# Kernel tuning notes

Hardware: AMD Instinct MI355X
Metric: run time of the kernel (lower is better)

## Reference

```python
import jax, jax.numpy as jnp
import numpy as np

NUM_FEATURES = 768
HIDDEN = 1024
BATCH = 8192
K = 32


def setup_inputs() -> dict:
    key = jax.random.key(0)
    k1, k2, k3, k4, k5 = jax.random.split(key, 5)
    white_features = jax.random.randint(k1, (BATCH, K), 0, NUM_FEATURES, dtype=jnp.int64 if jax.config.jax_enable_x64 else jnp.int32)
    black_features = jax.random.randint(k2, (BATCH, K), 0, NUM_FEATURES, dtype=jnp.int64 if jax.config.jax_enable_x64 else jnp.int32)
    stm = jax.random.randint(k3, (BATCH,), 0, 2, dtype=jnp.int32)
    ft_weight = jax.random.normal(k4, (NUM_FEATURES, HIDDEN), dtype=jnp.float32) * np.sqrt(2.0 / NUM_FEATURES)  # kaiming_normal fan_in, relu
    ft_bias = jnp.zeros((HIDDEN,), dtype=jnp.float32)
    out_weight = jax.random.normal(k5, (2 * HIDDEN,), dtype=jnp.float32) * 0.01
    out_bias = jnp.zeros((1,), dtype=jnp.float32)
    return {"white_features": white_features, "black_features": black_features, "stm": stm,
            "ft_weight": ft_weight, "ft_bias": ft_bias, "out_weight": out_weight, "out_bias": out_bias}


def _accumulate(features, ft_weight, ft_bias):
    # features: (B, K) indices, -1 means empty slot
    valid = (features >= 0)
    safe = jnp.clip(features, 0, None)
    w = jnp.take(ft_weight, safe, axis=0)  # (B, K, H)
    w = w * valid[..., None].astype(ft_weight.dtype)
    return ft_bias[None, :] + w.sum(axis=1)  # (B, H)


def _screlu(x):
    return jnp.square(jnp.clip(x, 0.0, 1.0))


def reference(white_features, black_features, stm, ft_weight, ft_bias, out_weight, out_bias):
    white_act = _screlu(_accumulate(white_features, ft_weight, ft_bias))
    black_act = _screlu(_accumulate(black_features, ft_weight, ft_bias))
    m = stm.astype(white_act.dtype)[:, None]  # (B, 1)
    us = white_act * (1.0 - m) + black_act * m
    them = black_act * (1.0 - m) + white_act * m
    combined = jnp.concatenate([us, them], axis=1)  # (B, 2H)
    return (combined * out_weight[None, :]).sum(axis=1) + out_bias[0]
```

## Files before the change

kernel.cpp:

```cpp
#include <hip/hip_runtime.h>

#define BATCH 8192
#define K 32
#define HID 1024
#define NF 768

#define QSCALE 3196.0f
#define QINV (1.0f / 3196.0f)
#define QMAX 1023

#define SLICES 16
#define SLICE_U 64
#define TAB_ROWS 769
#define SLICE_SHORTS (TAB_ROWS * SLICE_U)

#define WS_NEED (SLICES * BATCH * 4)

#define THREADS 1024

typedef __attribute__((ext_vector_type(2))) short s16x2;

static __device__ __forceinline__ s16x2 as_s16x2(unsigned u) {
    union { unsigned u; s16x2 v; } t; t.u = u; return t.v;
}

__global__ __launch_bounds__(THREADS, 4) void nnue_lds(
    const int* __restrict__ wf,
    const int* __restrict__ bfeat,
    const int* __restrict__ stm,
    const float* __restrict__ ftw,
    const float* __restrict__ ftb,
    const float* __restrict__ ow,
    float* __restrict__ part)
{
    __shared__ short tile[SLICE_SHORTS];

    const int blk = blockIdx.x;
    const int s   = blk & 15;
    const int g   = blk >> 4;
    const int tid = threadIdx.x;

    #pragma unroll 4
    for (int i = tid; i < TAB_ROWS * 16; i += THREADS) {
        const int row  = i >> 4;
        const int quad = i & 15;
        short4 q = {0, 0, 0, 0};
        if (row < NF) {
            const float4 w = *reinterpret_cast<const float4*>(
                ftw + (size_t)row * HID + s * SLICE_U + quad * 4);
            int qx = __float2int_rn(w.x * QSCALE);
            int qy = __float2int_rn(w.y * QSCALE);
            int qz = __float2int_rn(w.z * QSCALE);
            int qw = __float2int_rn(w.w * QSCALE);
            qx = max(-QMAX, min(QMAX, qx));
            qy = max(-QMAX, min(QMAX, qy));
            qz = max(-QMAX, min(QMAX, qz));
            qw = max(-QMAX, min(QMAX, qw));
            q.x = (short)qx; q.y = (short)qy; q.z = (short)qz; q.w = (short)qw;
        }
        *reinterpret_cast<short4*>(tile + row * SLICE_U + quad * 4) = q;
    }
    __syncthreads();

    const int a   = tid & 7;
    const int a8  = a * 8;
    const int sub = (tid >> 3) & 7;
    const int wv  = tid >> 6;
    const int U0  = s * SLICE_U + a8;

    float bias[8], owl[8], owh[8];
    {
        const float4 b0 = *reinterpret_cast<const float4*>(ftb + U0);
        const float4 b1 = *reinterpret_cast<const float4*>(ftb + U0 + 4);
        const float4 l0 = *reinterpret_cast<const float4*>(ow + U0);
        const float4 l1 = *reinterpret_cast<const float4*>(ow + U0 + 4);
        const float4 h0 = *reinterpret_cast<const float4*>(ow + HID + U0);
        const float4 h1 = *reinterpret_cast<const float4*>(ow + HID + U0 + 4);
        bias[0]=b0.x; bias[1]=b0.y; bias[2]=b0.z; bias[3]=b0.w;
        bias[4]=b1.x; bias[5]=b1.y; bias[6]=b1.z; bias[7]=b1.w;
        owl[0]=l0.x; owl[1]=l0.y; owl[2]=l0.z; owl[3]=l0.w;
        owl[4]=l1.x; owl[5]=l1.y; owl[6]=l1.z; owl[7]=l1.w;
        owh[0]=h0.x; owh[1]=h0.y; owh[2]=h0.z; owh[3]=h0.w;
        owh[4]=h1.x; owh[5]=h1.y; owh[6]=h1.z; owh[7]=h1.w;
    }

    #pragma unroll 1
    for (int pass = 0; pass < 4; ++pass) {
        const int e = g * 512 + pass * 128 + wv * 8 + sub;

        const uint4* wp = reinterpret_cast<const uint4*>(wf    + (size_t)e * K);
        const uint4* bp = reinterpret_cast<const uint4*>(bfeat + (size_t)e * K);
        uint4 iw[8], ib[8];
        #pragma unroll
        for (int q = 0; q < 8; ++q) { iw[q] = wp[q]; ib[q] = bp[q]; }
        const int m = stm[e];

        s16x2 accw[4] = {(s16x2){0,0},(s16x2){0,0},(s16x2){0,0},(s16x2){0,0}};
        s16x2 accb[4] = {(s16x2){0,0},(s16x2){0,0},(s16x2){0,0},(s16x2){0,0}};

        #define ROWACC(acc, idx)                                                   \
            do {                                                                   \
                const unsigned _r = min((unsigned)(idx), (unsigned)NF);            \
                const uint4 _x = *reinterpret_cast<const uint4*>(                  \
                    tile + _r * SLICE_U + a8);                                     \
                acc[0] += as_s16x2(_x.x);                                          \
                acc[1] += as_s16x2(_x.y);                                          \
                acc[2] += as_s16x2(_x.z);                                          \
                acc[3] += as_s16x2(_x.w);                                          \
            } while (0)

        #pragma unroll
        for (int q = 0; q < 8; ++q) {
            ROWACC(accw, iw[q].x);
            ROWACC(accb, ib[q].x);
            ROWACC(accw, iw[q].y);
            ROWACC(accb, ib[q].y);
            ROWACC(accw, iw[q].z);
            ROWACC(accb, ib[q].z);
            ROWACC(accw, iw[q].w);
            ROWACC(accb, ib[q].w);
        }

        float pw_lo = 0.f, pw_hi = 0.f, pb_lo = 0.f, pb_hi = 0.f;
        #pragma unroll
        for (int d = 0; d < 4; ++d) {
            const int j0 = 2 * d, j1 = 2 * d + 1;
            float xw0 = bias[j0] + (float)accw[d].x * QINV;
            float xw1 = bias[j1] + (float)accw[d].y * QINV;
            float xb0 = bias[j0] + (float)accb[d].x * QINV;
            float xb1 = bias[j1] + (float)accb[d].y * QINV;
            xw0 = fminf(fmaxf(xw0, 0.f), 1.f);  xw0 *= xw0;
            xw1 = fminf(fmaxf(xw1, 0.f), 1.f);  xw1 *= xw1;
            xb0 = fminf(fmaxf(xb0, 0.f), 1.f);  xb0 *= xb0;
            xb1 = fminf(fmaxf(xb1, 0.f), 1.f);  xb1 *= xb1;
            pw_lo += xw0 * owl[j0] + xw1 * owl[j1];
            pw_hi += xw0 * owh[j0] + xw1 * owh[j1];
            pb_lo += xb0 * owl[j0] + xb1 * owl[j1];
            pb_hi += xb0 * owh[j0] + xb1 * owh[j1];
        }
        float p = m ? (pb_lo + pw_hi) : (pw_lo + pb_hi);

        p += __shfl_xor(p, 1);
        p += __shfl_xor(p, 2);
        p += __shfl_xor(p, 4);

        if (a == 0)
            part[(size_t)s * BATCH + e] = p;
    }
}

__global__ __launch_bounds__(256) void finalize_kernel(const float* __restrict__ part,
                                                       const float* __restrict__ ob,
                                                       float* __restrict__ out) {
    const int e = blockIdx.x * 256 + threadIdx.x;
    float sum = ob[0];
    #pragma unroll
    for (int s = 0; s < SLICES; ++s)
        sum += part[(size_t)s * BATCH + e];
    out[e] = sum;
}

__global__ __launch_bounds__(256) void nnue_fwd_f32(
    const int* __restrict__ wf, const int* __restrict__ bfeat,
    const int* __restrict__ stm, const float* __restrict__ ftw,
    const float* __restrict__ ftb, const float* __restrict__ ow,
    const float* __restrict__ ob, float* __restrict__ out)
{
    __shared__ float sred[4];
    const int b   = blockIdx.x;
    const int tid = threadIdx.x;
    const int h0  = tid * 4;

    const int* wrow = wf + b * K;
    const int* brow = bfeat + b * K;

    float4 bias4 = *reinterpret_cast<const float4*>(ftb + h0);
    float4 accw = bias4, accb = bias4;

    #pragma unroll
    for (int k = 0; k < K; ++k) {
        const int iw = wrow[k];
        if (iw >= 0) {
            const float4 r = *reinterpret_cast<const float4*>(ftw + (size_t)iw * HID + h0);
            accw.x += r.x; accw.y += r.y; accw.z += r.z; accw.w += r.w;
        }
        const int ib = brow[k];
        if (ib >= 0) {
            const float4 r = *reinterpret_cast<const float4*>(ftw + (size_t)ib * HID + h0);
            accb.x += r.x; accb.y += r.y; accb.z += r.z; accb.w += r.w;
        }
    }

    #define SCRELU(x) ({ float _c = fminf(fmaxf((x), 0.0f), 1.0f); _c * _c; })
    float4 aw, ab;
    aw.x = SCRELU(accw.x); aw.y = SCRELU(accw.y); aw.z = SCRELU(accw.z); aw.w = SCRELU(accw.w);
    ab.x = SCRELU(accb.x); ab.y = SCRELU(accb.y); ab.z = SCRELU(accb.z); ab.w = SCRELU(accb.w);

    const int m = stm[b];
    const float4 us = m ? ab : aw;
    const float4 th = m ? aw : ab;

    const float4 ow0 = *reinterpret_cast<const float4*>(ow + h0);
    const float4 ow1 = *reinterpret_cast<const float4*>(ow + HID + h0);

    float p = us.x * ow0.x + us.y * ow0.y + us.z * ow0.z + us.w * ow0.w
            + th.x * ow1.x + th.y * ow1.y + th.z * ow1.z + th.w * ow1.w;

    #pragma unroll
    for (int off = 1; off < 64; off <<= 1)
        p += __shfl_xor(p, off);

    if ((tid & 63) == 0) sred[tid >> 6] = p;
    __syncthreads();
    if (tid == 0)
        out[b] = sred[0] + sred[1] + sred[2] + sred[3] + ob[0];
}

extern "C" void kernel_launch(void* const* d_in, const int* in_sizes, int n_in,
                              void* d_out, int out_size, void* d_ws, size_t ws_size,
                              hipStream_t stream) {
    const int*   wf    = (const int*)d_in[0];
    const int*   bfeat = (const int*)d_in[1];
    const int*   stm   = (const int*)d_in[2];
    const float* ftw   = (const float*)d_in[3];
    const float* ftb   = (const float*)d_in[4];
    const float* ow    = (const float*)d_in[5];
    const float* ob    = (const float*)d_in[6];

    if (ws_size >= (size_t)WS_NEED) {
        float* part = (float*)d_ws;
        nnue_lds<<<SLICES * 16, THREADS, 0, stream>>>(wf, bfeat, stm, ftw, ftb, ow, part);
        finalize_kernel<<<BATCH / 256, 256, 0, stream>>>(part, ob, (float*)d_out);
    } else {
        nnue_fwd_f32<<<BATCH, 256, 0, stream>>>(wf, bfeat, stm, ftw, ftb, ow, ob,
                                                (float*)d_out);
    }
}
```

Baseline: 28.19 us.

## Narrow LDS slices to 32 units and use more, smaller blocks

Splits the hidden dimension into 32 slices of 32 units instead of 16 of 64 and the batch into 32 groups. Blocks drop to 512 threads, giving 1024 blocks, each with a ~48KB LDS table and only 256 elements to process. Index loads are streamed per half-chunk instead of preloaded, and the bias and output weights are loaded after accumulation, to cut register pressure and allow 6 blocks per CU. The trade-off is twice as much total weight quantisation and table building across blocks, and twice as many partial sums for the finalize kernel to reduce.

```diff
diff --git a/kernel.cpp b/kernel.cpp
--- a/kernel.cpp
+++ b/kernel.cpp
@@ -9,14 +9,16 @@
 #define QINV (1.0f / 3196.0f)
 #define QMAX 1023
 
-#define SLICES 16
-#define SLICE_U 64
+#define SLICES 32
+#define SLICE_U 32
 #define TAB_ROWS 769
 #define SLICE_SHORTS (TAB_ROWS * SLICE_U)
 
+#define GROUPS 32
+#define GELEMS (BATCH / GROUPS)
+#define THREADS 512
+
 #define WS_NEED (SLICES * BATCH * 4)
-
-#define THREADS 1024
 
 typedef __attribute__((ext_vector_type(2))) short s16x2;
 
@@ -24,7 +26,7 @@
     union { unsigned u; s16x2 v; } t; t.u = u; return t.v;
 }
 
-__global__ __launch_bounds__(THREADS, 4) void nnue_lds(
+__global__ __launch_bounds__(THREADS, 6) void nnue_lds(
     const int* __restrict__ wf,
     const int* __restrict__ bfeat,
     const int* __restrict__ stm,
@@ -36,14 +38,14 @@
     __shared__ short tile[SLICE_SHORTS];
 
     const int blk = blockIdx.x;
-    const int s   = blk & 15;
-    const int g   = blk >> 4;
+    const int s   = blk & 31;
+    const int g   = blk >> 5;
     const int tid = threadIdx.x;
 
     #pragma unroll 4
-    for (int i = tid; i < TAB_ROWS * 16; i += THREADS) {
-        const int row  = i >> 4;
-        const int quad = i & 15;
+    for (int i = tid; i < TAB_ROWS * 8; i += THREADS) {
+        const int row  = i >> 3;
+        const int quad = i & 7;
         short4 q = {0, 0, 0, 0};
         if (row < NF) {
             const float4 w = *reinterpret_cast<const float4*>(
@@ -62,38 +64,18 @@
     }
     __syncthreads();
 
-    const int a   = tid & 7;
+    const int a   = tid & 3;
     const int a8  = a * 8;
-    const int sub = (tid >> 3) & 7;
+    const int sub = (tid >> 2) & 15;
     const int wv  = tid >> 6;
     const int U0  = s * SLICE_U + a8;
 
-    float bias[8], owl[8], owh[8];
-    {
-        const float4 b0 = *reinterpret_cast<const float4*>(ftb + U0);
-        const float4 b1 = *reinterpret_cast<const float4*>(ftb + U0 + 4);
-        const float4 l0 = *reinterpret_cast<const float4*>(ow + U0);
-        const float4 l1 = *reinterpret_cast<const float4*>(ow + U0 + 4);
-        const float4 h0 = *reinterpret_cast<const float4*>(ow + HID + U0);
-        const float4 h1 = *reinterpret_cast<const float4*>(ow + HID + U0 + 4);
-        bias[0]=b0.x; bias[1]=b0.y; bias[2]=b0.z; bias[3]=b0.w;
-        bias[4]=b1.x; bias[5]=b1.y; bias[6]=b1.z; bias[7]=b1.w;
-        owl[0]=l0.x; owl[1]=l0.y; owl[2]=l0.z; owl[3]=l0.w;
-        owl[4]=l1.x; owl[5]=l1.y; owl[6]=l1.z; owl[7]=l1.w;
-        owh[0]=h0.x; owh[1]=h0.y; owh[2]=h0.z; owh[3]=h0.w;
-        owh[4]=h1.x; owh[5]=h1.y; owh[6]=h1.z; owh[7]=h1.w;
-    }
-
     #pragma unroll 1
-    for (int pass = 0; pass < 4; ++pass) {
-        const int e = g * 512 + pass * 128 + wv * 8 + sub;
+    for (int pass = 0; pass < 2; ++pass) {
+        const int e = g * GELEMS + pass * 128 + wv * 16 + sub;
 
         const uint4* wp = reinterpret_cast<const uint4*>(wf    + (size_t)e * K);
         const uint4* bp = reinterpret_cast<const uint4*>(bfeat + (size_t)e * K);
-        uint4 iw[8], ib[8];
-        #pragma unroll
-        for (int q = 0; q < 8; ++q) { iw[q] = wp[q]; ib[q] = bp[q]; }
-        const int m = stm[e];
 
         s16x2 accw[4] = {(s16x2){0,0},(s16x2){0,0},(s16x2){0,0},(s16x2){0,0}};
         s16x2 accb[4] = {(s16x2){0,0},(s16x2){0,0},(s16x2){0,0},(s16x2){0,0}};
@@ -110,16 +92,31 @@
             } while (0)
 
         #pragma unroll
-        for (int q = 0; q < 8; ++q) {
-            ROWACC(accw, iw[q].x);
-            ROWACC(accb, ib[q].x);
-            ROWACC(accw, iw[q].y);
-            ROWACC(accb, ib[q].y);
-            ROWACC(accw, iw[q].z);
-            ROWACC(accb, ib[q].z);
-            ROWACC(accw, iw[q].w);
-            ROWACC(accb, ib[q].w);
-        }
+        for (int h = 0; h < 4; ++h) {
+            const uint4 w0 = wp[2 * h];
+            const uint4 w1 = wp[2 * h + 1];
+            const uint4 b0 = bp[2 * h];
+            const uint4 b1 = bp[2 * h + 1];
+            ROWACC(accw, w0.x); ROWACC(accb, b0.x);
+            ROWACC(accw, w0.y); ROWACC(accb, b0.y);
+            ROWACC(accw, w0.z); ROWACC(accb, b0.z);
+            ROWACC(accw, w0.w); ROWACC(accb, b0.w);
+            ROWACC(accw, w1.x); ROWACC(accb, b1.x);
+            ROWACC(accw, w1.y); ROWACC(accb, b1.y);
+            ROWACC(accw, w1.z); ROWACC(accb, b1.z);
+            ROWACC(accw, w1.w); ROWACC(accb, b1.w);
+        }
+
+        const int m = stm[e];
+        const float4 bi0 = *reinterpret_cast<const float4*>(ftb + U0);
+        const float4 bi1 = *reinterpret_cast<const float4*>(ftb + U0 + 4);
+        const float4 l0  = *reinterpret_cast<const float4*>(ow + U0);
+        const float4 l1  = *reinterpret_cast<const float4*>(ow + U0 + 4);
+        const float4 h0  = *reinterpret_cast<const float4*>(ow + HID + U0);
+        const float4 h1  = *reinterpret_cast<const float4*>(ow + HID + U0 + 4);
+        const float bias[8] = {bi0.x,bi0.y,bi0.z,bi0.w,bi1.x,bi1.y,bi1.z,bi1.w};
+        const float owl[8]  = {l0.x,l0.y,l0.z,l0.w,l1.x,l1.y,l1.z,l1.w};
+        const float owh[8]  = {h0.x,h0.y,h0.z,h0.w,h1.x,h1.y,h1.z,h1.w};
 
         float pw_lo = 0.f, pw_hi = 0.f, pb_lo = 0.f, pb_hi = 0.f;
         #pragma unroll
@@ -142,7 +139,6 @@
 
         p += __shfl_xor(p, 1);
         p += __shfl_xor(p, 2);
-        p += __shfl_xor(p, 4);
 
         if (a == 0)
             part[(size_t)s * BATCH + e] = p;
@@ -229,7 +225,8 @@
 
     if (ws_size >= (size_t)WS_NEED) {
         float* part = (float*)d_ws;
-        nnue_lds<<<SLICES * 16, THREADS, 0, stream>>>(wf, bfeat, stm, ftw, ftb, ow, part);
+        nnue_lds<<<SLICES * GROUPS, THREADS, 0, stream>>>(wf, bfeat, stm, ftw, ftb,
+                                                          ow, part);
         finalize_kernel<<<BATCH / 256, 256, 0, stream>>>(part, ob, (float*)d_out);
     } else {
         nnue_fwd_f32<<<BATCH, 256, 0, stream>>>(wf, bfeat, stm, ftw, ftb, ow, ob,
```

After: 29.04 us. 1.03x slower.

## Quantize table once in separate kernel and split batch between LDS and L2 paths

Applied to the files above, without the earlier changes.

Adds a pre-pass kernel that quantizes the feature-transformer weights to int16 once into workspace, so each block copies its slice into LDS instead of re-quantizing floats. Inside the main kernel, 14 of the 16 waves process the first 5376 positions via the LDS slice path. The remaining 2 waves per block handle the other positions directly from the global int16 table through L2, computing the full hidden width and writing final outputs. The aim is to cut the redundant quantization work and balance LDS-bound and L2-bound work, at the cost of an extra kernel launch and more global traffic for the L2 path.

```diff
diff --git a/kernel.cpp b/kernel.cpp
--- a/kernel.cpp
+++ b/kernel.cpp
@@ -9,14 +9,21 @@
 #define QINV (1.0f / 3196.0f)
 #define QMAX 1023
 
+#define TAB_ROWS 769
+#define TAB_BYTES (TAB_ROWS * HID * 2)
+
 #define SLICES 16
 #define SLICE_U 64
-#define TAB_ROWS 769
 #define SLICE_SHORTS (TAB_ROWS * SLICE_U)
 
-#define WS_NEED (SLICES * BATCH * 4)
-
 #define THREADS 1024
+#define GW 14
+#define E_LDS 5376
+#define GROUP_E 336
+#define PER_PASS 112
+#define L2_PER_BLK 11
+
+#define WS_NEED (TAB_BYTES + SLICES * BATCH * 4)
 
 typedef __attribute__((ext_vector_type(2))) short s16x2;
 
@@ -24,14 +31,35 @@
     union { unsigned u; s16x2 v; } t; t.u = u; return t.v;
 }
 
-__global__ __launch_bounds__(THREADS, 4) void nnue_lds(
+__global__ __launch_bounds__(256) void quantize_kernel(const float* __restrict__ ftw,
+                                                       short* __restrict__ tab) {
+    const int i = (blockIdx.x * 256 + threadIdx.x) * 4;
+    short4 q = {0, 0, 0, 0};
+    if (i < NF * HID) {
+        const float4 w = *reinterpret_cast<const float4*>(ftw + i);
+        int qx = __float2int_rn(w.x * QSCALE);
+        int qy = __float2int_rn(w.y * QSCALE);
+        int qz = __float2int_rn(w.z * QSCALE);
+        int qw = __float2int_rn(w.w * QSCALE);
+        qx = max(-QMAX, min(QMAX, qx));
+        qy = max(-QMAX, min(QMAX, qy));
+        qz = max(-QMAX, min(QMAX, qz));
+        qw = max(-QMAX, min(QMAX, qw));
+        q.x = (short)qx; q.y = (short)qy; q.z = (short)qz; q.w = (short)qw;
+    }
+    *reinterpret_cast<short4*>(tab + i) = q;
+}
+
+__global__ __launch_bounds__(THREADS, 4) void nnue_hybrid(
     const int* __restrict__ wf,
     const int* __restrict__ bfeat,
     const int* __restrict__ stm,
-    const float* __restrict__ ftw,
+    const short* __restrict__ tab,
     const float* __restrict__ ftb,
     const float* __restrict__ ow,
-    float* __restrict__ part)
+    const float* __restrict__ ob,
+    float* __restrict__ part,
+    float* __restrict__ out)
 {
     __shared__ short tile[SLICE_SHORTS];
 
@@ -40,112 +68,171 @@
     const int g   = blk >> 4;
     const int tid = threadIdx.x;
 
-    #pragma unroll 4
-    for (int i = tid; i < TAB_ROWS * 16; i += THREADS) {
-        const int row  = i >> 4;
-        const int quad = i & 15;
-        short4 q = {0, 0, 0, 0};
-        if (row < NF) {
-            const float4 w = *reinterpret_cast<const float4*>(
-                ftw + (size_t)row * HID + s * SLICE_U + quad * 4);
-            int qx = __float2int_rn(w.x * QSCALE);
-            int qy = __float2int_rn(w.y * QSCALE);
-            int qz = __float2int_rn(w.z * QSCALE);
-            int qw = __float2int_rn(w.w * QSCALE);
-            qx = max(-QMAX, min(QMAX, qx));
-            qy = max(-QMAX, min(QMAX, qy));
-            qz = max(-QMAX, min(QMAX, qz));
-            qw = max(-QMAX, min(QMAX, qw));
-            q.x = (short)qx; q.y = (short)qy; q.z = (short)qz; q.w = (short)qw;
-        }
-        *reinterpret_cast<short4*>(tile + row * SLICE_U + quad * 4) = q;
+    #pragma unroll 2
+    for (int i = tid; i < TAB_ROWS * 8; i += THREADS) {
+        const int row = i >> 3;
+        const int oct = i & 7;
+        *reinterpret_cast<uint4*>(tile + row * SLICE_U + oct * 8) =
+            *reinterpret_cast<const uint4*>(tab + (size_t)row * HID + s * SLICE_U + oct * 8);
     }
     __syncthreads();
 
-    const int a   = tid & 7;
-    const int a8  = a * 8;
-    const int sub = (tid >> 3) & 7;
-    const int wv  = tid >> 6;
-    const int U0  = s * SLICE_U + a8;
-
-    float bias[8], owl[8], owh[8];
-    {
-        const float4 b0 = *reinterpret_cast<const float4*>(ftb + U0);
-        const float4 b1 = *reinterpret_cast<const float4*>(ftb + U0 + 4);
-        const float4 l0 = *reinterpret_cast<const float4*>(ow + U0);
-        const float4 l1 = *reinterpret_cast<const float4*>(ow + U0 + 4);
-        const float4 h0 = *reinterpret_cast<const float4*>(ow + HID + U0);
-        const float4 h1 = *reinterpret_cast<const float4*>(ow + HID + U0 + 4);
-        bias[0]=b0.x; bias[1]=b0.y; bias[2]=b0.z; bias[3]=b0.w;
-        bias[4]=b1.x; bias[5]=b1.y; bias[6]=b1.z; bias[7]=b1.w;
-        owl[0]=l0.x; owl[1]=l0.y; owl[2]=l0.z; owl[3]=l0.w;
-        owl[4]=l1.x; owl[5]=l1.y; owl[6]=l1.z; owl[7]=l1.w;
-        owh[0]=h0.x; owh[1]=h0.y; owh[2]=h0.z; owh[3]=h0.w;
-        owh[4]=h1.x; owh[5]=h1.y; owh[6]=h1.z; owh[7]=h1.w;
-    }
-
-    #pragma unroll 1
-    for (int pass = 0; pass < 4; ++pass) {
-        const int e = g * 512 + pass * 128 + wv * 8 + sub;
-
-        const uint4* wp = reinterpret_cast<const uint4*>(wf    + (size_t)e * K);
-        const uint4* bp = reinterpret_cast<const uint4*>(bfeat + (size_t)e * K);
-        uint4 iw[8], ib[8];
-        #pragma unroll
-        for (int q = 0; q < 8; ++q) { iw[q] = wp[q]; ib[q] = bp[q]; }
-        const int m = stm[e];
-
-        s16x2 accw[4] = {(s16x2){0,0},(s16x2){0,0},(s16x2){0,0},(s16x2){0,0}};
-        s16x2 accb[4] = {(s16x2){0,0},(s16x2){0,0},(s16x2){0,0},(s16x2){0,0}};
-
-        #define ROWACC(acc, idx)                                                   \
-            do {                                                                   \
-                const unsigned _r = min((unsigned)(idx), (unsigned)NF);            \
-                const uint4 _x = *reinterpret_cast<const uint4*>(                  \
-                    tile + _r * SLICE_U + a8);                                     \
-                acc[0] += as_s16x2(_x.x);                                          \
-                acc[1] += as_s16x2(_x.y);                                          \
-                acc[2] += as_s16x2(_x.z);                                          \
-                acc[3] += as_s16x2(_x.w);                                          \
-            } while (0)
-
-        #pragma unroll
-        for (int q = 0; q < 8; ++q) {
-            ROWACC(accw, iw[q].x);
-            ROWACC(accb, ib[q].x);
-            ROWACC(accw, iw[q].y);
-            ROWACC(accb, ib[q].y);
-            ROWACC(accw, iw[q].z);
-            ROWACC(accb, ib[q].z);
-            ROWACC(accw, iw[q].w);
-            ROWACC(accb, ib[q].w);
-        }
-
-        float pw_lo = 0.f, pw_hi = 0.f, pb_lo = 0.f, pb_hi = 0.f;
-        #pragma unroll
-        for (int d = 0; d < 4; ++d) {
-            const int j0 = 2 * d, j1 = 2 * d + 1;
-            float xw0 = bias[j0] + (float)accw[d].x * QINV;
-            float xw1 = bias[j1] + (float)accw[d].y * QINV;
-            float xb0 = bias[j0] + (float)accb[d].x * QINV;
-            float xb1 = bias[j1] + (float)accb[d].y * QINV;
-            xw0 = fminf(fmaxf(xw0, 0.f), 1.f);  xw0 *= xw0;
-            xw1 = fminf(fmaxf(xw1, 0.f), 1.f);  xw1 *= xw1;
-            xb0 = fminf(fmaxf(xb0, 0.f), 1.f);  xb0 *= xb0;
-            xb1 = fminf(fmaxf(xb1, 0.f), 1.f);  xb1 *= xb1;
-            pw_lo += xw0 * owl[j0] + xw1 * owl[j1];
-            pw_hi += xw0 * owh[j0] + xw1 * owh[j1];
-            pb_lo += xb0 * owl[j0] + xb1 * owl[j1];
-            pb_hi += xb0 * owh[j0] + xb1 * owh[j1];
-        }
-        float p = m ? (pb_lo + pw_hi) : (pw_lo + pb_hi);
-
-        p += __shfl_xor(p, 1);
-        p += __shfl_xor(p, 2);
-        p += __shfl_xor(p, 4);
-
-        if (a == 0)
-            part[(size_t)s * BATCH + e] = p;
+    const int wv = tid >> 6;
+
+    if (wv < GW) {
+        const int a    = tid & 7;
+        const int a8   = a * 8;
+        const int sub  = (tid >> 3) & 7;
+        const int slot = wv * 8 + sub;
+        const int U0   = s * SLICE_U + a8;
+
+        float bias[8], owl[8], owh[8];
+        {
+            const float4 b0 = *reinterpret_cast<const float4*>(ftb + U0);
+            const float4 b1 = *reinterpret_cast<const float4*>(ftb + U0 + 4);
+            const float4 l0 = *reinterpret_cast<const float4*>(ow + U0);
+            const float4 l1 = *reinterpret_cast<const float4*>(ow + U0 + 4);
+            const float4 h0 = *reinterpret_cast<const float4*>(ow + HID + U0);
+            const float4 h1 = *reinterpret_cast<const float4*>(ow + HID + U0 + 4);
+            bias[0]=b0.x; bias[1]=b0.y; bias[2]=b0.z; bias[3]=b0.w;
+            bias[4]=b1.x; bias[5]=b1.y; bias[6]=b1.z; bias[7]=b1.w;
+            owl[0]=l0.x; owl[1]=l0.y; owl[2]=l0.z; owl[3]=l0.w;
+            owl[4]=l1.x; owl[5]=l1.y; owl[6]=l1.z; owl[7]=l1.w;
+            owh[0]=h0.x; owh[1]=h0.y; owh[2]=h0.z; owh[3]=h0.w;
+            owh[4]=h1.x; owh[5]=h1.y; owh[6]=h1.z; owh[7]=h1.w;
+        }
+
+        #pragma unroll 1
+        for (int pass = 0; pass < 3; ++pass) {
+            const int e = g * GROUP_E + pass * PER_PASS + slot;
+
+            const uint4* wp = reinterpret_cast<const uint4*>(wf    + (size_t)e * K);
+            const uint4* bp = reinterpret_cast<const uint4*>(bfeat + (size_t)e * K);
+
+            s16x2 accw[4] = {(s16x2){0,0},(s16x2){0,0},(s16x2){0,0},(s16x2){0,0}};
+            s16x2 accb[4] = {(s16x2){0,0},(s16x2){0,0},(s16x2){0,0},(s16x2){0,0}};
+
+            #define ROWACC(acc, idx)                                               \
+                do {                                                               \
+                    const unsigned _r = min((unsigned)(idx), (unsigned)NF);        \
+                    const uint4 _x = *reinterpret_cast<const uint4*>(              \
+                        tile + _r * SLICE_U + a8);                                 \
+                    acc[0] += as_s16x2(_x.x);                                      \
+                    acc[1] += as_s16x2(_x.y);                                      \
+                    acc[2] += as_s16x2(_x.z);                                      \
+                    acc[3] += as_s16x2(_x.w);                                      \
+                } while (0)
+
+            #pragma unroll
+            for (int h = 0; h < 4; ++h) {
+                const uint4 w0 = wp[2 * h];
+                const uint4 w1 = wp[2 * h + 1];
+                const uint4 b0 = bp[2 * h];
+                const uint4 b1 = bp[2 * h + 1];
+                ROWACC(accw, w0.x); ROWACC(accb, b0.x);
+                ROWACC(accw, w0.y); ROWACC(accb, b0.y);
+                ROWACC(accw, w0.z); ROWACC(accb, b0.z);
+                ROWACC(accw, w0.w); ROWACC(accb, b0.w);
+                ROWACC(accw, w1.x); ROWACC(accb, b1.x);
+                ROWACC(accw, w1.y); ROWACC(accb, b1.y);
+                ROWACC(accw, w1.z); ROWACC(accb, b1.z);
+                ROWACC(accw, w1.w); ROWACC(accb, b1.w);
+            }
+
+            const int m = stm[e];
+            float pw_lo = 0.f, pw_hi = 0.f, pb_lo = 0.f, pb_hi = 0.f;
+            #pragma unroll
+            for (int d = 0; d < 4; ++d) {
+                const int j0 = 2 * d, j1 = 2 * d + 1;
+                float xw0 = bias[j0] + (float)accw[d].x * QINV;
+                float xw1 = bias[j1] + (float)accw[d].y * QINV;
+                float xb0 = bias[j0] + (float)accb[d].x * QINV;
+                float xb1 = bias[j1] + (float)accb[d].y * QINV;
+                xw0 = fminf(fmaxf(xw0, 0.f), 1.f);  xw0 *= xw0;
+                xw1 = fminf(fmaxf(xw1, 0.f), 1.f);  xw1 *= xw1;
+                xb0 = fminf(fmaxf(xb0, 0.f), 1.f);  xb0 *= xb0;
+                xb1 = fminf(fmaxf(xb1, 0.f), 1.f);  xb1 *= xb1;
+                pw_lo += xw0 * owl[j0] + xw1 * owl[j1];
+                pw_hi += xw0 * owh[j0] + xw1 * owh[j1];
+                pb_lo += xb0 * owl[j0] + xb1 * owl[j1];
+                pb_hi += xb0 * owh[j0] + xb1 * owh[j1];
+            }
+            float p = m ? (pb_lo + pw_hi) : (pw_lo + pb_hi);
+
+            p += __shfl_xor(p, 1);
+            p += __shfl_xor(p, 2);
+            p += __shfl_xor(p, 4);
+
+            if (a == 0)
+                part[(size_t)s * BATCH + e] = p;
+        }
+    } else {
+        const int lane = tid & 63;
+        const int wl   = wv - GW;
+        const int u0   = lane * 16;
+        const int nel  = wl ? (L2_PER_BLK - 6) : 6;
+        const int eb   = E_LDS + blk * L2_PER_BLK + (wl ? 6 : 0);
+
+        for (int el = 0; el < nel; ++el) {
+            const int e = eb + el;
+            const int* wrow = wf    + (size_t)e * K;
+            const int* brow = bfeat + (size_t)e * K;
+
+            s16x2 aw[8], ab[8];
+            #pragma unroll
+            for (int d = 0; d < 8; ++d) { aw[d] = (s16x2){0,0}; ab[d] = (s16x2){0,0}; }
+
+            #pragma unroll 4
+            for (int k = 0; k < K; ++k) {
+                const unsigned riw = min((unsigned)wrow[k], (unsigned)NF);
+                const unsigned rib = min((unsigned)brow[k], (unsigned)NF);
+                const short* rw = tab + (size_t)riw * HID + u0;
+                const short* rb = tab + (size_t)rib * HID + u0;
+                const uint4 x0 = *reinterpret_cast<const uint4*>(rw);
+                const uint4 x1 = *reinterpret_cast<const uint4*>(rw + 8);
+                const uint4 y0 = *reinterpret_cast<const uint4*>(rb);
+                const uint4 y1 = *reinterpret_cast<const uint4*>(rb + 8);
+                aw[0] += as_s16x2(x0.x); aw[1] += as_s16x2(x0.y);
+                aw[2] += as_s16x2(x0.z); aw[3] += as_s16x2(x0.w);
+                aw[4] += as_s16x2(x1.x); aw[5] += as_s16x2(x1.y);
+                aw[6] += as_s16x2(x1.z); aw[7] += as_s16x2(x1.w);
+                ab[0] += as_s16x2(y0.x); ab[1] += as_s16x2(y0.y);
+                ab[2] += as_s16x2(y0.z); ab[3] += as_s16x2(y0.w);
+                ab[4] += as_s16x2(y1.x); ab[5] += as_s16x2(y1.y);
+                ab[6] += as_s16x2(y1.z); ab[7] += as_s16x2(y1.w);
+            }
+
+            const int m = stm[e];
+            float pw_lo = 0.f, pw_hi = 0.f, pb_lo = 0.f, pb_hi = 0.f;
+            #pragma unroll
+            for (int d = 0; d < 8; ++d) {
+                const int j0 = u0 + 2 * d, j1 = u0 + 2 * d + 1;
+                const float b0 = ftb[j0], b1 = ftb[j1];
+                float xw0 = b0 + (float)aw[d].x * QINV;
+                float xw1 = b1 + (float)aw[d].y * QINV;
+                float xb0 = b0 + (float)ab[d].x * QINV;
+                float xb1 = b1 + (float)ab[d].y * QINV;
+                xw0 = fminf(fmaxf(xw0, 0.f), 1.f);  xw0 *= xw0;
+                xw1 = fminf(fmaxf(xw1, 0.f), 1.f);  xw1 *= xw1;
+                xb0 = fminf(fmaxf(xb0, 0.f), 1.f);  xb0 *= xb0;
+                xb1 = fminf(fmaxf(xb1, 0.f), 1.f);  xb1 *= xb1;
+                pw_lo += xw0 * ow[j0] + xw1 * ow[j1];
+                pw_hi += xw0 * ow[HID + j0] + xw1 * ow[HID + j1];
+                pb_lo += xb0 * ow[j0] + xb1 * ow[j1];
+                pb_hi += xb0 * ow[HID + j0] + xb1 * ow[HID + j1];
+            }
+            float p = m ? (pb_lo + pw_hi) : (pw_lo + pb_hi);
+
+            p += __shfl_xor(p, 1);
+            p += __shfl_xor(p, 2);
+            p += __shfl_xor(p, 4);
+            p += __shfl_xor(p, 8);
+            p += __shfl_xor(p, 16);
+            p += __shfl_xor(p, 32);
+
+            if (lane == 0)
+                out[e] = p + ob[0];
+        }
     }
 }
 
@@ -153,11 +240,13 @@
                                                        const float* __restrict__ ob,
                                                        float* __restrict__ out) {
     const int e = blockIdx.x * 256 + threadIdx.x;
-    float sum = ob[0];
-    #pragma unroll
-    for (int s = 0; s < SLICES; ++s)
-        sum += part[(size_t)s * BATCH + e];
-    out[e] = sum;
+    if (e < E_LDS) {
+        float sum = ob[0];
+        #pragma unroll
+        for (int s = 0; s < SLICES; ++s)
+            sum += part[(size_t)s * BATCH + e];
+        out[e] = sum;
+    }
 }
 
 __global__ __launch_bounds__(256) void nnue_fwd_f32(
@@ -228,9 +317,13 @@
     const float* ob    = (const float*)d_in[6];
 
     if (ws_size >= (size_t)WS_NEED) {
-        float* part = (float*)d_ws;
-        nnue_lds<<<SLICES * 16, THREADS, 0, stream>>>(wf, bfeat, stm, ftw, ftb, ow, part);
-        finalize_kernel<<<BATCH / 256, 256, 0, stream>>>(part, ob, (float*)d_out);
+        short* tab  = (short*)d_ws;
+        float* part = (float*)((char*)d_ws + TAB_BYTES);
+        quantize_kernel<<<TAB_ROWS, 256, 0, stream>>>(ftw, tab);
+        nnue_hybrid<<<SLICES * 16, THREADS, 0, stream>>>(wf, bfeat, stm, tab, ftb,
+                                                         ow, ob, part, (float*)d_out);
+        finalize_kernel<<<(E_LDS + 255) / 256, 256, 0, stream>>>(part, ob,
+                                                                 (float*)d_out);
     } else {
         nnue_fwd_f32<<<BATCH, 256, 0, stream>>>(wf, bfeat, stm, ftw, ftb, ow, ob,
                                                 (float*)d_out);
```

New measurement: 56.10 us. +99.0%, slower.
